# Performance work log

Measured on AMD Instinct MI355X. Metric: run time of the kernel, lower is better.

## Reference

```python
import jax, jax.numpy as jnp
import numpy as np

B, S1, S2, DV = 64, 1024, 1024, 256

def setup_inputs() -> dict:
    key0 = jax.random.key(0)
    k1, k2, k3, k4, k5 = jax.random.split(key0, 5)
    return {
        "x": jax.random.normal(k1, (B, S1, 3), dtype=jnp.float32),
        "key": jax.random.normal(k2, (B, S2, 3), dtype=jnp.float32),
        "value": jax.random.normal(k3, (B, S2, DV), dtype=jnp.float32),
        "W": jax.random.normal(k4, (1, 6), dtype=jnp.float32) * (1.0 / np.sqrt(6.0)),
        "b": jax.random.normal(k5, (1,), dtype=jnp.float32) * 0.1,
    }

def reference(x, key, value, W, b):
    # Original: cat([x_rep, key_rep], -1) @ W^T + b == x @ W[:, :3]^T + key @ W[:, 3:]^T + b.
    # This avoids materializing the (B, S1, S2, 6) expanded tensor while computing identical math.
    w_x = W[0, :3]                      # (3,)
    w_k = W[0, 3:]                      # (3,)
    sx = jnp.einsum('bif,f->bi', x, w_x)      # (B, S1)
    sk = jnp.einsum('bjf,f->bj', key, w_k)    # (B, S2)
    scores = sx[:, :, None] + sk[:, None, :] + b[0]   # (B, S1, S2)
    attn = jax.nn.softmax(scores, axis=-1)            # softmax over S2
    return jnp.einsum('bij,bjd->bid', attn, value)    # (B, S1, DV)
```

## Files before the change

### kernel.cpp

```cpp
#include <hip/hip_runtime.h>


#define NB 64
#define S1V 1024
#define S2V 1024
#define DVV 256
#define NCHUNK 8
#define JPC (S2V / NCHUNK)


__global__ __launch_bounds__(256) void k_softmax(const float* __restrict__ key,
                                                 const float* __restrict__ W,
                                                 float* __restrict__ p) {
    const int b = blockIdx.x;
    const int t = threadIdx.x;
    const float wk0 = W[3], wk1 = W[4], wk2 = W[5];

    const float4* k4 = (const float4*)(key + (size_t)b * S2V * 3);
    float4 a = k4[3 * t + 0];
    float4 c = k4[3 * t + 1];
    float4 d = k4[3 * t + 2];
    float sk0 = a.x * wk0 + a.y * wk1 + a.z * wk2;
    float sk1 = a.w * wk0 + c.x * wk1 + c.y * wk2;
    float sk2 = c.z * wk0 + c.w * wk1 + d.x * wk2;
    float sk3 = d.y * wk0 + d.z * wk1 + d.w * wk2;

    float m = fmaxf(fmaxf(sk0, sk1), fmaxf(sk2, sk3));
    for (int off = 32; off; off >>= 1) m = fmaxf(m, __shfl_xor(m, off));
    __shared__ float redm[4];
    const int wave = t >> 6, lane = t & 63;
    if (lane == 0) redm[wave] = m;
    __syncthreads();
    m = fmaxf(fmaxf(redm[0], redm[1]), fmaxf(redm[2], redm[3]));

    float e0 = __expf(sk0 - m), e1 = __expf(sk1 - m);
    float e2 = __expf(sk2 - m), e3 = __expf(sk3 - m);
    float s = e0 + e1 + e2 + e3;
    for (int off = 32; off; off >>= 1) s += __shfl_xor(s, off);
    __shared__ float reds[4];
    if (lane == 0) reds[wave] = s;
    __syncthreads();
    s = reds[0] + reds[1] + reds[2] + reds[3];

    const float inv = 1.0f / s;
    float4 out4 = make_float4(e0 * inv, e1 * inv, e2 * inv, e3 * inv);
    ((float4*)(p + (size_t)b * S2V))[t] = out4;
}

__global__ __launch_bounds__(256) void k_pv(const float* __restrict__ value,
                                            const float* __restrict__ p,
                                            float* __restrict__ partial) {
    const int b = blockIdx.x >> 3;
    const int chunk = blockIdx.x & (NCHUNK - 1);
    const int t = threadIdx.x;
    const int wave = t >> 6, lane = t & 63;

    __shared__ float p_lds[JPC];
    if (t < JPC) p_lds[t] = p[(size_t)b * S2V + chunk * JPC + t];
    __syncthreads();

    const float4* v4 = (const float4*)(value + (size_t)b * S2V * DVV);
    float4 acc = make_float4(0.f, 0.f, 0.f, 0.f);
    const int jbase = chunk * JPC + wave * 32;
    #pragma unroll 8
    for (int i = 0; i < 32; ++i) {
        const int j = jbase + i;
        const float pj = p_lds[wave * 32 + i];
        float4 v = v4[(size_t)j * 64 + lane];
        acc.x += pj * v.x;
        acc.y += pj * v.y;
        acc.z += pj * v.z;
        acc.w += pj * v.w;
    }

    __shared__ float4 accl[256];
    accl[t] = acc;
    __syncthreads();
    if (wave == 0) {
        float4 r0 = accl[lane];
        float4 r1 = accl[64 + lane];
        float4 r2 = accl[128 + lane];
        float4 r3 = accl[192 + lane];
        r0.x += r1.x + r2.x + r3.x;
        r0.y += r1.y + r2.y + r3.y;
        r0.z += r1.z + r2.z + r3.z;
        r0.w += r1.w + r2.w + r3.w;
        ((float4*)(partial + ((size_t)b * NCHUNK + chunk) * DVV))[lane] = r0;
    }
}

__global__ __launch_bounds__(256) void k_reduce(const float* __restrict__ partial,
                                                float* __restrict__ row) {
    const int b = blockIdx.x;
    const int t = threadIdx.x;
    float acc = 0.f;
    #pragma unroll
    for (int c = 0; c < NCHUNK; ++c)
        acc += partial[((size_t)b * NCHUNK + c) * DVV + t];
    row[(size_t)b * DVV + t] = acc;
}

__global__ __launch_bounds__(256) void k_bcast(const float* __restrict__ row,
                                               float* __restrict__ out) {
    const int b = blockIdx.x >> 7;
    const int rt = blockIdx.x & 127;
    const int t = threadIdx.x;
    const int d4 = t & 63;
    const int rsub = t >> 6;

    float4 r = ((const float4*)(row + (size_t)b * DVV))[d4];
    float4* out4 = (float4*)(out + ((size_t)b * S1V + (size_t)rt * 8) * DVV);
    out4[(size_t)rsub * 64 + d4] = r;
    out4[(size_t)(rsub + 4) * 64 + d4] = r;
}

extern "C" void kernel_launch(void* const* d_in, const int* in_sizes, int n_in,
                              void* d_out, int out_size, void* d_ws, size_t ws_size,
                              hipStream_t stream) {
    const float* key   = (const float*)d_in[1];
    const float* value = (const float*)d_in[2];
    const float* W     = (const float*)d_in[3];
    float* out = (float*)d_out;

    float* p       = (float*)d_ws;
    float* partial = (float*)((char*)d_ws + 262144);
    float* row     = (float*)((char*)d_ws + 786432);

    k_softmax<<<NB, 256, 0, stream>>>(key, W, p);
    k_pv<<<NB * NCHUNK, 256, 0, stream>>>(value, p, partial);
    k_reduce<<<NB, 256, 0, stream>>>(partial, row);
    k_bcast<<<NB * 128, 256, 0, stream>>>(row, out);
}
```

Before: 125.3 us.

## Fuse softmax into PV kernel and reduce partials inside broadcast kernel

Each PV block now recomputes the full key softmax in registers and keeps only its chunk of probabilities in LDS, so the separate softmax kernel and its global probability buffer go away. The chunk-partial reduction moves into the broadcast kernel, which also uses nontemporal stores for the large output write. The chunk count doubles to spread the value read across more blocks. Four launches become two, at the cost of redundant softmax work per block and every broadcast block re-reducing the same partials.

```diff
diff --git a/kernel.cpp b/kernel.cpp
--- a/kernel.cpp
+++ b/kernel.cpp
@@ -5,30 +5,37 @@
 #define S1V 1024
 #define S2V 1024
 #define DVV 256
-#define NCHUNK 8
+#define NCHUNK 16
 #define JPC (S2V / NCHUNK)
 
+typedef float nf4 __attribute__((ext_vector_type(4)));
 
-__global__ __launch_bounds__(256) void k_softmax(const float* __restrict__ key,
-                                                 const float* __restrict__ W,
-                                                 float* __restrict__ p) {
-    const int b = blockIdx.x;
-    const int t = threadIdx.x;
+
+__global__ __launch_bounds__(256) void k_pv(const float* __restrict__ key,
+                                            const float* __restrict__ value,
+                                            const float* __restrict__ W,
+                                            float* __restrict__ partial) {
+    const int b     = blockIdx.x >> 4;
+    const int chunk = blockIdx.x & (NCHUNK - 1);
+    const int t     = threadIdx.x;
+    const int wave  = t >> 6, lane = t & 63;
+
     const float wk0 = W[3], wk1 = W[4], wk2 = W[5];
 
     const float4* k4 = (const float4*)(key + (size_t)b * S2V * 3);
     float4 a = k4[3 * t + 0];
     float4 c = k4[3 * t + 1];
     float4 d = k4[3 * t + 2];
-    float sk0 = a.x * wk0 + a.y * wk1 + a.z * wk2;
-    float sk1 = a.w * wk0 + c.x * wk1 + c.y * wk2;
-    float sk2 = c.z * wk0 + c.w * wk1 + d.x * wk2;
-    float sk3 = d.y * wk0 + d.z * wk1 + d.w * wk2;
+    float sk0 = fmaf(a.x, wk0, fmaf(a.y, wk1, a.z * wk2));
+    float sk1 = fmaf(a.w, wk0, fmaf(c.x, wk1, c.y * wk2));
+    float sk2 = fmaf(c.z, wk0, fmaf(c.w, wk1, d.x * wk2));
+    float sk3 = fmaf(d.y, wk0, fmaf(d.z, wk1, d.w * wk2));
+
+    __shared__ float redm[4], reds[4];
 
     float m = fmaxf(fmaxf(sk0, sk1), fmaxf(sk2, sk3));
+    #pragma unroll
     for (int off = 32; off; off >>= 1) m = fmaxf(m, __shfl_xor(m, off));
-    __shared__ float redm[4];
-    const int wave = t >> 6, lane = t & 63;
     if (lane == 0) redm[wave] = m;
     __syncthreads();
     m = fmaxf(fmaxf(redm[0], redm[1]), fmaxf(redm[2], redm[3]));
@@ -36,41 +43,35 @@
     float e0 = __expf(sk0 - m), e1 = __expf(sk1 - m);
     float e2 = __expf(sk2 - m), e3 = __expf(sk3 - m);
     float s = e0 + e1 + e2 + e3;
+    #pragma unroll
     for (int off = 32; off; off >>= 1) s += __shfl_xor(s, off);
-    __shared__ float reds[4];
     if (lane == 0) reds[wave] = s;
     __syncthreads();
     s = reds[0] + reds[1] + reds[2] + reds[3];
-
     const float inv = 1.0f / s;
-    float4 out4 = make_float4(e0 * inv, e1 * inv, e2 * inv, e3 * inv);
-    ((float4*)(p + (size_t)b * S2V))[t] = out4;
-}
-
-__global__ __launch_bounds__(256) void k_pv(const float* __restrict__ value,
-                                            const float* __restrict__ p,
-                                            float* __restrict__ partial) {
-    const int b = blockIdx.x >> 3;
-    const int chunk = blockIdx.x & (NCHUNK - 1);
-    const int t = threadIdx.x;
-    const int wave = t >> 6, lane = t & 63;
 
     __shared__ float p_lds[JPC];
-    if (t < JPC) p_lds[t] = p[(size_t)b * S2V + chunk * JPC + t];
+    const int tlo = chunk * (JPC / 4);
+    if (t >= tlo && t < tlo + JPC / 4) {
+        const int q = (t - tlo) * 4;
+        p_lds[q + 0] = e0 * inv;
+        p_lds[q + 1] = e1 * inv;
+        p_lds[q + 2] = e2 * inv;
+        p_lds[q + 3] = e3 * inv;
+    }
     __syncthreads();
 
     const float4* v4 = (const float4*)(value + (size_t)b * S2V * DVV);
+    const int jbase = chunk * JPC + wave * (JPC / 4);
     float4 acc = make_float4(0.f, 0.f, 0.f, 0.f);
-    const int jbase = chunk * JPC + wave * 32;
-    #pragma unroll 8
-    for (int i = 0; i < 32; ++i) {
-        const int j = jbase + i;
-        const float pj = p_lds[wave * 32 + i];
-        float4 v = v4[(size_t)j * 64 + lane];
-        acc.x += pj * v.x;
-        acc.y += pj * v.y;
-        acc.z += pj * v.z;
-        acc.w += pj * v.w;
+    #pragma unroll
+    for (int i = 0; i < JPC / 4; ++i) {
+        const float pj = p_lds[wave * (JPC / 4) + i];
+        float4 v = v4[(size_t)(jbase + i) * 64 + lane];
+        acc.x = fmaf(pj, v.x, acc.x);
+        acc.y = fmaf(pj, v.y, acc.y);
+        acc.z = fmaf(pj, v.z, acc.z);
+        acc.w = fmaf(pj, v.w, acc.w);
     }
 
     __shared__ float4 accl[256];
@@ -89,29 +90,37 @@
     }
 }
 
-__global__ __launch_bounds__(256) void k_reduce(const float* __restrict__ partial,
-                                                float* __restrict__ row) {
-    const int b = blockIdx.x;
-    const int t = threadIdx.x;
-    float acc = 0.f;
-    #pragma unroll
-    for (int c = 0; c < NCHUNK; ++c)
-        acc += partial[((size_t)b * NCHUNK + c) * DVV + t];
-    row[(size_t)b * DVV + t] = acc;
-}
-
-__global__ __launch_bounds__(256) void k_bcast(const float* __restrict__ row,
-                                               float* __restrict__ out) {
-    const int b = blockIdx.x >> 7;
-    const int rt = blockIdx.x & 127;
-    const int t = threadIdx.x;
-    const int d4 = t & 63;
+__global__ __launch_bounds__(256) void k_out(const float* __restrict__ partial,
+                                             float* __restrict__ out) {
+    const int b    = blockIdx.x >> 7;
+    const int rt   = blockIdx.x & 127;
+    const int t    = threadIdx.x;
+    const int d4   = t & 63;
     const int rsub = t >> 6;
 
-    float4 r = ((const float4*)(row + (size_t)b * DVV))[d4];
-    float4* out4 = (float4*)(out + ((size_t)b * S1V + (size_t)rt * 8) * DVV);
-    out4[(size_t)rsub * 64 + d4] = r;
-    out4[(size_t)(rsub + 4) * 64 + d4] = r;
+    const float4* pp = (const float4*)(partial + (size_t)b * NCHUNK * DVV);
+    float4 acc = make_float4(0.f, 0.f, 0.f, 0.f);
+    #pragma unroll
+    for (int c = rsub * 4; c < rsub * 4 + 4; ++c) {
+        float4 v = pp[c * 64 + d4];
+        acc.x += v.x; acc.y += v.y; acc.z += v.z; acc.w += v.w;
+    }
+    __shared__ float4 accl[256];
+    accl[t] = acc;
+    __syncthreads();
+    float4 r = accl[d4];
+    float4 r1 = accl[64 + d4];
+    float4 r2 = accl[128 + d4];
+    float4 r3 = accl[192 + d4];
+    r.x += r1.x + r2.x + r3.x;
+    r.y += r1.y + r2.y + r3.y;
+    r.z += r1.z + r2.z + r3.z;
+    r.w += r1.w + r2.w + r3.w;
+
+    nf4 rv = { r.x, r.y, r.z, r.w };
+    nf4* out4 = (nf4*)(out + ((size_t)b * S1V + (size_t)rt * 8) * DVV);
+    __builtin_nontemporal_store(rv, &out4[(size_t)rsub * 64 + d4]);
+    __builtin_nontemporal_store(rv, &out4[(size_t)(rsub + 4) * 64 + d4]);
 }
 
 extern "C" void kernel_launch(void* const* d_in, const int* in_sizes, int n_in,
@@ -122,12 +131,8 @@
     const float* W     = (const float*)d_in[3];
     float* out = (float*)d_out;
 
-    float* p       = (float*)d_ws;
-    float* partial = (float*)((char*)d_ws + 262144);
-    float* row     = (float*)((char*)d_ws + 786432);
+    float* partial = (float*)d_ws;
 
-    k_softmax<<<NB, 256, 0, stream>>>(key, W, p);
-    k_pv<<<NB * NCHUNK, 256, 0, stream>>>(value, p, partial);
-    k_reduce<<<NB, 256, 0, stream>>>(partial, row);
-    k_bcast<<<NB * 128, 256, 0, stream>>>(row, out);
+    k_pv<<<NB * NCHUNK, 256, 0, stream>>>(key, value, W, partial);
+    k_out<<<NB * 128, 256, 0, stream>>>(partial, out);
 }
```

Result: faster. 119.8 us (median of 2 runs) (-4.4%).
